# Optimization experiments

Hardware: AMD Instinct MI355X
Metric: run time of the kernel (lower is better)

Reference implementation:

```python
import jax, jax.numpy as jnp
import numpy as np
from jax import lax

B, S, D, H = 8, 1024, 512, 8
K = 25  # moving-average kernel
EPS = 1e-6


def setup_inputs() -> dict:
    key = jax.random.key(0)
    ks = jax.random.split(key, 8)

    def dense_w(k, din, dout):
        return (jax.random.normal(k, (din, dout), jnp.float32) / np.sqrt(din).astype(np.float32))

    return {
        "x": jax.random.normal(ks[0], (B, S, D), jnp.float32),
        "wq": dense_w(ks[1], D, D), "bq": jnp.zeros((D,), jnp.float32),
        "wk": dense_w(ks[2], D, D), "bk": jnp.zeros((D,), jnp.float32),
        "wv": dense_w(ks[3], D, D), "bv": jnp.zeros((D,), jnp.float32),
        "wo": dense_w(ks[4], D, D), "bo": jnp.zeros((D,), jnp.float32),
        "w1": dense_w(ks[5], D, 4 * D), "b1": jnp.zeros((4 * D,), jnp.float32),
        "w2": dense_w(ks[6], 4 * D, D), "b2": jnp.zeros((D,), jnp.float32),
        "g1": jnp.ones((D,), jnp.float32), "be1": jnp.zeros((D,), jnp.float32),
        "g2": jnp.ones((D,), jnp.float32), "be2": jnp.zeros((D,), jnp.float32),
        "g3": jnp.ones((D,), jnp.float32), "be3": jnp.zeros((D,), jnp.float32),
        "num_heads": H,
    }


def _moving_avg(x):
    # TF AveragePooling1D(pool=K, stride=1, padding='same'): divisor excludes padding.
    s = lax.reduce_window(x, 0.0, lax.add, (1, K, 1), (1, 1, 1), 'SAME')
    cnt = lax.reduce_window(jnp.ones((1, x.shape[1], 1), x.dtype), 0.0, lax.add,
                            (1, K, 1), (1, 1, 1), 'SAME')
    return s / cnt


def _layernorm(x, g, b):
    m = jnp.mean(x, -1, keepdims=True)
    v = jnp.var(x, -1, keepdims=True)
    return (x - m) * jax.lax.rsqrt(v + EPS) * g + b


def _auto_correlation(x, wq, bq, wk, bk, wv, bv, wo, bo, num_heads):
    b, s, d = x.shape
    dp = d // num_heads
    def split_heads(t):
        return t.reshape(b, s, num_heads, dp).transpose(0, 2, 1, 3)  # [B,H,S,dp]
    q = split_heads(x @ wq + bq)
    k = split_heads(x @ wk + bk)
    v = split_heads(x @ wv + bv)
    # Faithful to source: rfft over innermost (depth) axis, fft_length = 2*S.
    qf = jnp.fft.rfft(q, n=2 * s, axis=-1)
    kf = jnp.fft.rfft(k, n=2 * s, axis=-1)
    corr = jnp.fft.irfft(qf * jnp.conj(kf), n=2 * s, axis=-1)[..., :s]  # [B,H,S,S]
    scale = 1.0 / np.sqrt(dp).astype(np.float32)
    attn = jax.nn.softmax(scale * corr, axis=-1)
    out = jnp.einsum('bhst,bhtd->bhsd', attn, v)
    out = out.transpose(0, 2, 1, 3).reshape(b, s, d)
    return out @ wo + bo


def reference(x, wq, bq, wk, bk, wv, bv, wo, bo, w1, b1, w2, b2,
              g1, be1, g2, be2, g3, be3, num_heads):
    trend_init = _moving_avg(x)
    seasonal_init = x - trend_init
    attn_out = _auto_correlation(seasonal_init, wq, bq, wk, bk, wv, bv, wo, bo, num_heads)
    out1 = _layernorm(attn_out + seasonal_init, g1, be1)
    ffn = jax.nn.relu(out1 @ w1 + b1) @ w2 + b2
    seasonal_out = _layernorm(out1 + ffn, g2, be2) + seasonal_init
    trend2 = _moving_avg(seasonal_out)
    seasonal_final = seasonal_out - trend2
    x_out = seasonal_final + (trend2 + trend_init)
    return _layernorm(x_out, g3, be3)
```

## Files before the change

### kernel.cpp

```cpp
#include <hip/hip_runtime.h>
#include <cstdint>


typedef float f32x4 __attribute__((ext_vector_type(4)));
typedef __bf16 bf16x8 __attribute__((ext_vector_type(8)));
typedef _Float16 h2t __attribute__((ext_vector_type(2)));
typedef unsigned short u16;
typedef unsigned int u32;
typedef u32 u32x4 __attribute__((ext_vector_type(4)));

__device__ __forceinline__ u16 f2bf(float f) {
  unsigned int u = __float_as_uint(f);
  u = (u + 0x7FFFu + ((u >> 16) & 1u)) >> 16;
  return (u16)u;
}

__device__ __forceinline__ float bf2f(u16 b) { return __uint_as_float((u32)b << 16); }

__device__ __forceinline__ u16 f2h(float f) {
  _Float16 hv = (_Float16)f;
  u16 b;
  __builtin_memcpy(&b, &hv, 2);
  return b;
}

__device__ __forceinline__ float dot2h(u32 qp, u32 kp_, float c) {
#if __has_builtin(__builtin_amdgcn_fdot2)
  return __builtin_amdgcn_fdot2(__builtin_bit_cast(h2t, qp),
                                __builtin_bit_cast(h2t, kp_), c, false);
#else
  h2t q = __builtin_bit_cast(h2t, qp), k = __builtin_bit_cast(h2t, kp_);
  c = fmaf((float)q.x, (float)k.x, c);
  return fmaf((float)q.y, (float)k.y, c);
#endif
}

__device__ __forceinline__ void gload_lds16(const void* g, void* l) {
  __builtin_amdgcn_global_load_lds((__attribute__((address_space(1))) void*)g,
                                   (__attribute__((address_space(3))) void*)l,
                                   16, 0, 0);
}

__global__ __launch_bounds__(256) void movavg_kernel(
    const float* __restrict__ x, u16* __restrict__ seas_bf,
    u16* __restrict__ a64, float* __restrict__ srow) {
  int blk = blockIdx.x;
  int sc = blk & 127, b = blk >> 7;
  int d = threadIdx.x * 2;
  const float* xb = x + (size_t)b * 1024 * 512 + d;
  int s0 = sc * 8;
  int lo = max(s0 - 12, 0), hi = min(s0 + 12, 1023);
  float sx = 0.f, sy = 0.f;
  for (int j = lo; j <= hi; ++j) {
    float2 v = *(const float2*)&xb[(size_t)j * 512];
    sx += v.x;
    sy += v.y;
  }
  float ax = 0.f, ay = 0.f;
#pragma unroll
  for (int s = s0; s < s0 + 8; ++s) {
    int l2 = max(s - 12, 0), h2 = min(s + 12, 1023);
    float invc = 1.f / (float)(h2 - l2 + 1);
    float2 xv = *(const float2*)&xb[(size_t)s * 512];
    float sex = xv.x - sx * invc;
    float sey = xv.y - sy * invc;
    size_t idx = (size_t)(b * 1024 + s) * 512 + d;
    u32 pk = (u32)f2bf(sex) | ((u32)f2bf(sey) << 16);
    *(u32*)&seas_bf[idx] = pk;
    if (s < 64) *(u32*)&a64[(size_t)(b * 64 + s) * 512 + d] = pk;
    ax += sex;
    ay += sey;
    if (s - 12 >= 0) {
      float2 v = *(const float2*)&xb[(size_t)(s - 12) * 512];
      sx -= v.x;
      sy -= v.y;
    }
    if (s + 13 <= 1023) {
      float2 v = *(const float2*)&xb[(size_t)(s + 13) * 512];
      sx += v.x;
      sy += v.y;
    }
  }
  atomicAdd(&srow[b * 512 + d], ax);
  atomicAdd(&srow[b * 512 + d + 1], ay);
}

__global__ __launch_bounds__(256) void weights_prep_kernel(
    const float* __restrict__ wq, const float* __restrict__ wk,
    const float* __restrict__ wv, const float* __restrict__ wo,
    const float* __restrict__ w1, const float* __restrict__ w2,
    const float* __restrict__ bq, const float* __restrict__ bk,
    u16* __restrict__ wqkt, u16* __restrict__ wvt, u16* __restrict__ wot,
    u16* __restrict__ w1t, u16* __restrict__ w2t, float* __restrict__ qkbias) {
  __shared__ float tile[32][33];
  int i = blockIdx.x;
  int tx = threadIdx.x, ty = threadIdx.y;
  if (i >= 3072) {
    int idx = (i - 3072) * 256 + ty * 32 + tx;
    qkbias[idx] = idx < 512 ? bq[idx] : bk[idx - 512];
    return;
  }
  const float* src;
  u16* dst;
  int R, C, bx, by;
  if (i < 1024) {
    int w = i >> 8, l = i & 255;
    src = (w == 0 ? wq : w == 1 ? wk : w == 2 ? wv : wo);
    dst = (w == 0 ? wqkt : w == 1 ? wqkt + 512 * 512 : w == 2 ? wvt : wot);
    R = 512; C = 512; bx = l & 15; by = l >> 4;
  } else if (i < 2048) {
    int l = i - 1024;
    src = w1; dst = w1t; R = 512; C = 2048; bx = l & 15; by = l >> 4;
  } else {
    int l = i - 2048;
    src = w2; dst = w2t; R = 2048; C = 512; bx = l & 63; by = l >> 6;
  }
  int r0 = bx * 32, c0 = by * 32;
#pragma unroll
  for (int k = 0; k < 4; ++k)
    tile[ty + 8 * k][tx] = src[(size_t)(r0 + ty + 8 * k) * C + c0 + tx];
  __syncthreads();
#pragma unroll
  for (int k = 0; k < 4; ++k)
    dst[(size_t)(c0 + ty + 8 * k) * R + r0 + tx] = f2bf(tile[tx][ty + 8 * k]);
}

__global__ __launch_bounds__(256) void vsum_kernel(
    const float* __restrict__ srow, const float* __restrict__ wv,
    const float* __restrict__ bv, float* __restrict__ vsum) {
  int blk = blockIdx.x;
  int b = blk >> 1;
  int n = (blk & 1) * 256 + threadIdx.x;
  float acc = 0.f;
  for (int k = 0; k < 512; ++k) acc += srow[b * 512 + k] * wv[(size_t)k * 512 + n];
  vsum[b * 512 + n] = acc + 1024.f * bv[n];
}

template <int RELU, int OMODE, int KSPLIT>
__global__ __launch_bounds__(256, 6) void gemm_bf16_kernel(
    const u16* __restrict__ A, const u16* __restrict__ Bt,
    const float* __restrict__ bias, void* __restrict__ Cv, void* __restrict__ Cv2,
    int M, int N, int K) {
  constexpr int BK = 32;
  __shared__ u16 As[2][128 * BK];
  __shared__ u16 Bs[2][64 * BK];
  const int tid = threadIdx.x;
  const int wid = tid >> 6, lane = tid & 63;
  const int wm = wid >> 1, wn = wid & 1;
  const int la = lane & 15, lg = lane >> 4;
  int nwg = gridDim.x * gridDim.y;
  int lin = blockIdx.y * gridDim.x + blockIdx.x;
  int swz = (lin & 7) * (nwg >> 3) + (lin >> 3);
  int bx = swz / gridDim.y;
  int by = swz % gridDim.y;
  const int row0 = bx * 128, col0 = by * 64;
  const int z = (KSPLIT > 1) ? (int)blockIdx.z : 0;
  const int kbeg = z * (K / KSPLIT);
  const int ksteps = (K / KSPLIT) / BK;
  f32x4 acc[4][2] = {};

  auto stage = [&](int buf, int k0) {
    {
      int p = tid, r = p >> 2, cg = (p & 3) ^ ((r >> 1) & 3);
      gload_lds16(A + (size_t)(row0 + r) * K + k0 + cg * 8, ((char*)As[buf]) + p * 16);
    }
    {
      int p = tid + 256, r = p >> 2, cg = (p & 3) ^ ((r >> 1) & 3);
      gload_lds16(A + (size_t)(row0 + r) * K + k0 + cg * 8, ((char*)As[buf]) + p * 16);
    }
    {
      int p = tid, r = p >> 2, cg = (p & 3) ^ ((r >> 1) & 3);
      gload_lds16(Bt + (size_t)(col0 + r) * K + k0 + cg * 8, ((char*)Bs[buf]) + p * 16);
    }
  };

  stage(0, kbeg);
  __syncthreads();
  for (int t = 0; t < ksteps; ++t) {
    const int cur = t & 1;
    if (t + 1 < ksteps) stage(cur ^ 1, kbeg + (t + 1) * BK);
    bf16x8 af[4], bfr[2];
#pragma unroll
    for (int m = 0; m < 4; ++m) {
      int r = wm * 64 + m * 16 + la;
      int cp = lg ^ ((r >> 1) & 3);
      af[m] = *(const bf16x8*)(((const char*)As[cur]) + r * 64 + cp * 16);
    }
#pragma unroll
    for (int n = 0; n < 2; ++n) {
      int r = wn * 32 + n * 16 + la;
      int cp = lg ^ ((r >> 1) & 3);
      bfr[n] = *(const bf16x8*)(((const char*)Bs[cur]) + r * 64 + cp * 16);
    }
    __builtin_amdgcn_s_setprio(1);
#pragma unroll
    for (int m = 0; m < 4; ++m)
#pragma unroll
      for (int n = 0; n < 2; ++n)
        acc[m][n] = __builtin_amdgcn_mfma_f32_16x16x32_bf16(af[m], bfr[n], acc[m][n], 0, 0, 0);
    __builtin_amdgcn_s_setprio(0);
    __syncthreads();
  }

  void* Cout = (z == 0) ? Cv : Cv2;
#pragma unroll
  for (int m = 0; m < 4; ++m) {
    int r = row0 + wm * 64 + m * 16 + lg * 4;
#pragma unroll
    for (int n = 0; n < 2; ++n) {
      int cc = col0 + wn * 32 + n * 16 + la;
      float bvv = (z == 0) ? bias[cc] : 0.f;
#pragma unroll
      for (int j = 0; j < 4; ++j) {
        float v = acc[m][n][j] + bvv;
        if (RELU) v = fmaxf(v, 0.f);
        if constexpr (OMODE == 0) {
          ((float*)Cout)[(size_t)(r + j) * N + cc] = v;
        } else if constexpr (OMODE == 1) {
          ((u16*)Cout)[(size_t)(r + j) * N + cc] = f2bf(v);
        } else if constexpr (OMODE == 2) {
          ((u16*)Cout)[(size_t)(r + j) * N + cc] = f2h(v);
        } else {
          int rr = r + j;
          int bb = rr >> 6, tt = rr & 63, hh = cc >> 6, dd = cc & 63;
          ((u16*)Cout)[(((size_t)bb * 8 + hh) * 64 + dd) * 64 + tt] = f2bf(v);
        }
      }
    }
  }
}

__global__ __launch_bounds__(256) void attn_mfma_kernel(
    const u16* __restrict__ qk, const u16* __restrict__ v64t,
    const float* __restrict__ vsum, u16* __restrict__ attn_bf) {
  __shared__ u32 qE[32][64];
  __shared__ u32 qO[32][64];
  __shared__ u32 kp[32][32];
  __shared__ u16 coef[32][64];
  __shared__ u16 vtt[64][64];
  __shared__ float zc[32];
  __shared__ float Vs[64];
  int bid = blockIdx.x;
  int scnk = bid & 31, h = (bid >> 5) & 7, b = bid >> 8;
  int tid = threadIdx.x, wid = tid >> 6, lane = tid & 63;
  int bh = b * 8 + h;

  {
    int p = tid, r = p >> 3, cc = p & 7;
    gload_lds16(v64t + ((size_t)bh * 4096 + r * 64 + ((cc ^ (r & 7)) * 8)),
                ((char*)vtt) + p * 16);
    p = tid + 256; r = p >> 3; cc = p & 7;
    gload_lds16(v64t + ((size_t)bh * 4096 + r * 64 + ((cc ^ (r & 7)) * 8)),
                ((char*)vtt) + p * 16);
  }
  *(f32x4*)&qE[tid >> 3][32 + ((tid & 7) << 2)] = f32x4{};
  {
    int s = tid >> 3, c = tid & 7;
    size_t grow = ((size_t)(b * 1024 + scnk * 32 + s)) * 1024 + h * 64;
    *(f32x4*)&qE[s][c * 4] = *(const f32x4*)&qk[grow + c * 8];
    *(f32x4*)&kp[s][c * 4] = *(const f32x4*)&qk[grow + 512 + c * 8];
  }
  if (tid < 64) Vs[tid] = vsum[b * 512 + h * 64 + tid];
  __syncthreads();
  for (int j2 = tid; j2 < 1024; j2 += 256) {
    int s = j2 >> 5, j = j2 & 31;
    u32 a = qE[s][j], b2 = qE[s][j + 1];
    qO[s][j] = (a >> 16) | (b2 << 16);
    qO[s][j + 32] = 0;
  }
  __syncthreads();
  for (int i = 0; i < 8; ++i) {
    int s = wid * 8 + i;
    u32x4 kk4[8];
#pragma unroll
    for (int u = 0; u < 8; ++u) kk4[u] = *(const u32x4*)&kp[s][u * 4];
    int t = lane, sel = t & 1;
    const u32* qptr = (sel ? qO[s] : qE[s]) + (t >> 1);
    float c = 0.f;
#pragma unroll
    for (int u = 0; u < 8; ++u) {
#pragma unroll
      for (int v = 0; v < 4; ++v) c = dot2h(qptr[u * 4 + v], kk4[u][v], c);
    }
    float sc = c * 0.125f;
    float mx = fmaxf(sc, 0.f);
#pragma unroll
    for (int off = 32; off >= 1; off >>= 1) mx = fmaxf(mx, __shfl_xor(mx, off));
    float w = __expf(sc - mx), wz = __expf(-mx);
    float sw = w;
#pragma unroll
    for (int off = 32; off >= 1; off >>= 1) sw += __shfl_xor(sw, off);
    float inv = 1.f / (sw + 960.f * wz);
    *(u16*)(((char*)&coef[s][0]) + ((2 * t) ^ ((s & 7) << 4))) = f2bf((w - wz) * inv);
    if (lane == 0) zc[s] = wz * inv;
  }
  __syncthreads();
  {
    int sm = wid >> 1, nh = wid & 1;
    int la = lane & 15, lg = lane >> 4;
    int r = sm * 16 + la;
    int n0 = nh * 32 + la, n1 = nh * 32 + 16 + la;
    f32x4 acc0 = {}, acc1 = {};
#pragma unroll
    for (int ks = 0; ks < 2; ++ks) {
      int lr = ks * 4 + lg;
      bf16x8 af = *(const bf16x8*)(((const char*)coef) + r * 128 + ((lr ^ (r & 7)) << 4));
      bf16x8 bf0 = *(const bf16x8*)(((const char*)vtt) + n0 * 128 + ((lr ^ (n0 & 7)) << 4));
      bf16x8 bf1 = *(const bf16x8*)(((const char*)vtt) + n1 * 128 + ((lr ^ (n1 & 7)) << 4));
      acc0 = __builtin_amdgcn_mfma_f32_16x16x32_bf16(af, bf0, acc0, 0, 0, 0);
      acc1 = __builtin_amdgcn_mfma_f32_16x16x32_bf16(af, bf1, acc1, 0, 0, 0);
    }
    int srl0 = sm * 16 + lg * 4;
    int srow0 = b * 1024 + scnk * 32 + srl0;
    float vs0 = Vs[nh * 32 + la], vs1 = Vs[nh * 32 + 16 + la];
#pragma unroll
    for (int j = 0; j < 4; ++j) {
      float zcv = zc[srl0 + j];
      size_t rb = (size_t)(srow0 + j) * 512 + h * 64;
      attn_bf[rb + nh * 32 + la] = f2bf(acc0[j] + zcv * vs0);
      attn_bf[rb + nh * 32 + 16 + la] = f2bf(acc1[j] + zcv * vs1);
    }
  }
}

__device__ __forceinline__ void block_reduce_2(float& a, float& b, float* sbuf) {
  int tid = threadIdx.x, wid = tid >> 6, lane = tid & 63;
#pragma unroll
  for (int off = 32; off >= 1; off >>= 1) {
    a += __shfl_xor(a, off);
    b += __shfl_xor(b, off);
  }
  if (lane == 0) {
    sbuf[wid] = a;
    sbuf[4 + wid] = b;
  }
  __syncthreads();
  a = sbuf[0] + sbuf[1] + sbuf[2] + sbuf[3];
  b = sbuf[4] + sbuf[5] + sbuf[6] + sbuf[7];
  __syncthreads();
}

__global__ __launch_bounds__(256) void ln_res_kernel(
    const u16* __restrict__ xa, const u16* __restrict__ xb,
    u16* __restrict__ res_out,
    const float* __restrict__ g, const float* __restrict__ be) {
  __shared__ float sbuf[8];
  int row = blockIdx.x, tid = threadIdx.x;
  int d = tid * 2;
  size_t base = (size_t)row * 512 + d;
  u32 pa = *(const u32*)&xa[base];
  u32 pb = *(const u32*)&xb[base];
  u32 pr = *(const u32*)&res_out[base];
  float v0 = bf2f((u16)pa) + bf2f((u16)pb) + bf2f((u16)pr);
  float v1 = bf2f((u16)(pa >> 16)) + bf2f((u16)(pb >> 16)) + bf2f((u16)(pr >> 16));
  float s = v0 + v1, q = v0 * v0 + v1 * v1;
  block_reduce_2(s, q, sbuf);
  float mean = s * (1.f / 512.f);
  float var = q * (1.f / 512.f) - mean * mean;
  float rs = rsqrtf(var + 1e-6f);
  float2 gg = *(const float2*)&g[d];
  float2 bb = *(const float2*)&be[d];
  float o0 = (v0 - mean) * rs * gg.x + bb.x;
  float o1 = (v1 - mean) * rs * gg.y + bb.y;
  *(u32*)&res_out[base] = (u32)f2bf(o0) | ((u32)f2bf(o1) << 16);
}

__global__ __launch_bounds__(256) void final_kernel(
    const u16* __restrict__ out1, const u16* __restrict__ fa,
    const u16* __restrict__ fb, const float* __restrict__ x,
    const float* __restrict__ g2, const float* __restrict__ be2,
    const float* __restrict__ g3, const float* __restrict__ be3,
    float* __restrict__ out) {
  __shared__ float sbuf[8];
  int row = blockIdx.x, tid = threadIdx.x;
  int d = tid * 2;
  size_t base = (size_t)row * 512 + d;
  u32 po = *(const u32*)&out1[base];
  u32 pa = *(const u32*)&fa[base];
  u32 pb = *(const u32*)&fb[base];
  float t0 = bf2f((u16)po) + bf2f((u16)pa) + bf2f((u16)pb);
  float t1 = bf2f((u16)(po >> 16)) + bf2f((u16)(pa >> 16)) + bf2f((u16)(pb >> 16));
  float s = t0 + t1, q = t0 * t0 + t1 * t1;
  block_reduce_2(s, q, sbuf);
  float mean = s * (1.f / 512.f);
  float var = q * (1.f / 512.f) - mean * mean;
  float rs = rsqrtf(var + 1e-6f);
  float2 g2v = *(const float2*)&g2[d];
  float2 b2v = *(const float2*)&be2[d];
  float2 xv = *(const float2*)&x[base];
  float y0 = (t0 - mean) * rs * g2v.x + b2v.x + xv.x;
  float y1 = (t1 - mean) * rs * g2v.y + b2v.y + xv.y;
  s = y0 + y1;
  q = y0 * y0 + y1 * y1;
  block_reduce_2(s, q, sbuf);
  mean = s * (1.f / 512.f);
  var = q * (1.f / 512.f) - mean * mean;
  rs = rsqrtf(var + 1e-6f);
  float2 g3v = *(const float2*)&g3[d];
  float2 b3v = *(const float2*)&be3[d];
  float2 o = make_float2((y0 - mean) * rs * g3v.x + b3v.x,
                         (y1 - mean) * rs * g3v.y + b3v.y);
  *(float2*)&out[base] = o;
}

extern "C" void kernel_launch(void* const* d_in, const int* in_sizes, int n_in,
                              void* d_out, int out_size, void* d_ws, size_t ws_size,
                              hipStream_t stream) {
  const float* x = (const float*)d_in[0];
  const float* wq = (const float*)d_in[1];
  const float* bq = (const float*)d_in[2];
  const float* wk = (const float*)d_in[3];
  const float* bk = (const float*)d_in[4];
  const float* wv = (const float*)d_in[5];
  const float* bv = (const float*)d_in[6];
  const float* wo = (const float*)d_in[7];
  const float* bo = (const float*)d_in[8];
  const float* w1 = (const float*)d_in[9];
  const float* b1 = (const float*)d_in[10];
  const float* w2 = (const float*)d_in[11];
  const float* b2 = (const float*)d_in[12];
  const float* g1 = (const float*)d_in[13];
  const float* be1 = (const float*)d_in[14];
  const float* g2 = (const float*)d_in[15];
  const float* be2 = (const float*)d_in[16];
  const float* g3 = (const float*)d_in[17];
  const float* be3 = (const float*)d_in[18];
  float* out = (float*)d_out;

  const size_t MS = 8192ull * 512ull;
  float* srow = (float*)d_ws;
  float* vsumb = srow + 4096;
  float* qkbias = vsumb + 4096;
  u16* qk_f16 = (u16*)(qkbias + 1024);
  u16* hidden = qk_f16 + 8192ull * 1024;
  u16* seas_bf = hidden + 8192ull * 2048;
  u16* attn_bf = seas_bf + MS;
  u16* wo0 = attn_bf + MS;
  u16* wo1 = wo0 + MS;
  u16* v64t = wo1 + MS;
  u16* a64_bf = v64t + 512 * 512;
  u16* wqkt = a64_bf + 512 * 512;
  u16* wvt = wqkt + 1024 * 512;
  u16* wot = wvt + 512 * 512;
  u16* w1t = wot + 512 * 512;
  u16* w2t = w1t + 2048ull * 512;
  u16* ff0 = qk_f16;
  u16* ff1 = ff0 + MS;

  hipMemsetAsync(srow, 0, 4096 * sizeof(float), stream);
  weights_prep_kernel<<<3076, dim3(32, 8), 0, stream>>>(
      wq, wk, wv, wo, w1, w2, bq, bk, wqkt, wvt, wot, w1t, w2t, qkbias);

  movavg_kernel<<<1024, 256, 0, stream>>>(x, seas_bf, a64_bf, srow);
  vsum_kernel<<<16, 256, 0, stream>>>(srow, wv, bv, vsumb);

  gemm_bf16_kernel<0, 2, 1><<<dim3(64, 16), 256, 0, stream>>>(
      seas_bf, wqkt, qkbias, qk_f16, nullptr, 8192, 1024, 512);
  gemm_bf16_kernel<0, 3, 1><<<dim3(4, 8), 256, 0, stream>>>(
      a64_bf, wvt, bv, v64t, nullptr, 512, 512, 512);

  attn_mfma_kernel<<<2048, 256, 0, stream>>>(qk_f16, v64t, vsumb, attn_bf);

  gemm_bf16_kernel<0, 1, 2><<<dim3(64, 8, 2), 256, 0, stream>>>(
      attn_bf, wot, bo, wo0, wo1, 8192, 512, 512);
  ln_res_kernel<<<8192, 256, 0, stream>>>(wo0, wo1, seas_bf, g1, be1);

  gemm_bf16_kernel<1, 1, 1><<<dim3(64, 32), 256, 0, stream>>>(
      seas_bf, w1t, b1, hidden, nullptr, 8192, 2048, 512);
  gemm_bf16_kernel<0, 1, 2><<<dim3(64, 8, 2), 256, 0, stream>>>(
      hidden, w2t, b2, ff0, ff1, 8192, 512, 2048);

  final_kernel<<<8192, 256, 0, stream>>>(seas_bf, ff0, ff1, x, g2, be2, g3, be3, out);
}
```

Before: 214.8 us.

## Replace bf16 GEMMs with 256x128-tile, 8-wave, triple-buffered pipelined kernel

The large GEMMs (QK projection, output projection, FFN up/down) move to a new kernel with 512 threads, 256x128 output tiles, a 64-wide K step split into two 32-wide halves, and a three-stage LDS ring. The ring is managed with explicit vmcnt waits and raw barriers so global-to-LDS loads run two steps ahead of the MFMAs. Larger tiles raise arithmetic intensity and cut redundant operand loads. The cost is fewer workgroups: only 256 blocks for the QK GEMM and 256 for the split-K N=512 GEMMs on a 256-CU part, with one block per CU. The small V GEMM gets its own specialised kernel with the transposed store.

```diff
diff --git a/kernel.cpp b/kernel.cpp
--- a/kernel.cpp
+++ b/kernel.cpp
@@ -137,10 +137,117 @@
 }
 
 template <int RELU, int OMODE, int KSPLIT>
-__global__ __launch_bounds__(256, 6) void gemm_bf16_kernel(
+__global__ __launch_bounds__(512, 1) void gemm8p_kernel(
     const u16* __restrict__ A, const u16* __restrict__ Bt,
     const float* __restrict__ bias, void* __restrict__ Cv, void* __restrict__ Cv2,
     int M, int N, int K) {
+  __shared__ u16 As[3][2][256 * 32];
+  __shared__ u16 Bs[3][2][128 * 32];
+  const int tid = threadIdx.x;
+  const int wid = tid >> 6, lane = tid & 63;
+  const int wm = wid >> 2, wn = wid & 3;
+  const int la = lane & 15, lg = lane >> 4;
+  int nwg = gridDim.x * gridDim.y;
+  int lin = blockIdx.y * gridDim.x + blockIdx.x;
+  int swz = (lin & 7) * (nwg >> 3) + (lin >> 3);
+  int bx = swz / gridDim.y, by = swz % gridDim.y;
+  const int row0 = bx * 256, col0 = by * 128;
+  const int z = (KSPLIT > 1) ? (int)blockIdx.z : 0;
+  const int kbeg = z * (K / KSPLIT);
+  const int nt = (K / KSPLIT) / 64;
+  f32x4 acc[8][2] = {};
+
+  auto stageh = [&](int buf, int h, int k0) {
+    int kh = k0 + h * 32;
+    {
+      int p = tid, r = p >> 2, cg = (p & 3) ^ ((r >> 1) & 3);
+      gload_lds16(A + (size_t)(row0 + r) * K + kh + cg * 8,
+                  ((char*)&As[buf][h][0]) + p * 16);
+    }
+    {
+      int p = tid + 512, r = p >> 2, cg = (p & 3) ^ ((r >> 1) & 3);
+      gload_lds16(A + (size_t)(row0 + r) * K + kh + cg * 8,
+                  ((char*)&As[buf][h][0]) + p * 16);
+    }
+    {
+      int p = tid, r = p >> 2, cg = (p & 3) ^ ((r >> 1) & 3);
+      gload_lds16(Bt + (size_t)(col0 + r) * K + kh + cg * 8,
+                  ((char*)&Bs[buf][h][0]) + p * 16);
+    }
+  };
+
+  stageh(0, 0, kbeg);
+  stageh(0, 1, kbeg);
+  stageh(1, 0, kbeg + 64);
+  stageh(1, 1, kbeg + 64);
+  asm volatile("s_waitcnt vmcnt(6)" ::: "memory");
+  __builtin_amdgcn_s_barrier();
+  __builtin_amdgcn_sched_barrier(0);
+
+  for (int t = 0; t < nt; ++t) {
+    const int buf = t % 3;
+    const int nbuf = (t + 2) % 3;
+    const bool pre = (t + 2 < nt);
+#pragma unroll
+    for (int h = 0; h < 2; ++h) {
+      bf16x8 af[8], bf[2];
+#pragma unroll
+      for (int mf = 0; mf < 8; ++mf) {
+        int r = wm * 128 + mf * 16 + la;
+        int cp = lg ^ ((r >> 1) & 3);
+        af[mf] = *(const bf16x8*)&As[buf][h][r * 32 + cp * 8];
+      }
+#pragma unroll
+      for (int nf = 0; nf < 2; ++nf) {
+        int r = wn * 32 + nf * 16 + la;
+        int cp = lg ^ ((r >> 1) & 3);
+        bf[nf] = *(const bf16x8*)&Bs[buf][h][r * 32 + cp * 8];
+      }
+      if (pre) stageh(nbuf, h, kbeg + (t + 2) * 64);
+      __builtin_amdgcn_sched_barrier(0);
+      __builtin_amdgcn_s_barrier();
+      __builtin_amdgcn_s_setprio(1);
+#pragma unroll
+      for (int mf = 0; mf < 8; ++mf)
+#pragma unroll
+        for (int nf = 0; nf < 2; ++nf)
+          acc[mf][nf] = __builtin_amdgcn_mfma_f32_16x16x32_bf16(af[mf], bf[nf], acc[mf][nf], 0, 0, 0);
+      __builtin_amdgcn_s_setprio(0);
+      __builtin_amdgcn_sched_barrier(0);
+      if (h == 0) __builtin_amdgcn_s_barrier();
+    }
+    if (pre)
+      asm volatile("s_waitcnt vmcnt(6)" ::: "memory");
+    else if (t + 1 < nt)
+      asm volatile("s_waitcnt vmcnt(0)" ::: "memory");
+    __builtin_amdgcn_s_barrier();
+    __builtin_amdgcn_sched_barrier(0);
+  }
+
+  void* Cout = (z == 0) ? Cv : Cv2;
+#pragma unroll
+  for (int mf = 0; mf < 8; ++mf) {
+    int r = row0 + wm * 128 + mf * 16 + lg * 4;
+#pragma unroll
+    for (int nf = 0; nf < 2; ++nf) {
+      int cc = col0 + wn * 32 + nf * 16 + la;
+      float bvv = (z == 0) ? bias[cc] : 0.f;
+#pragma unroll
+      for (int j = 0; j < 4; ++j) {
+        float v = acc[mf][nf][j] + bvv;
+        if (RELU) v = fmaxf(v, 0.f);
+        if constexpr (OMODE == 1)
+          ((u16*)Cout)[(size_t)(r + j) * N + cc] = f2bf(v);
+        else
+          ((u16*)Cout)[(size_t)(r + j) * N + cc] = f2h(v);
+      }
+    }
+  }
+}
+
+__global__ __launch_bounds__(256, 6) void gemm_v_kernel(
+    const u16* __restrict__ A, const u16* __restrict__ Bt,
+    const float* __restrict__ bias, u16* __restrict__ Cv, int M, int N, int K) {
   constexpr int BK = 32;
   __shared__ u16 As[2][128 * BK];
   __shared__ u16 Bs[2][64 * BK];
@@ -148,15 +255,8 @@
   const int wid = tid >> 6, lane = tid & 63;
   const int wm = wid >> 1, wn = wid & 1;
   const int la = lane & 15, lg = lane >> 4;
-  int nwg = gridDim.x * gridDim.y;
-  int lin = blockIdx.y * gridDim.x + blockIdx.x;
-  int swz = (lin & 7) * (nwg >> 3) + (lin >> 3);
-  int bx = swz / gridDim.y;
-  int by = swz % gridDim.y;
-  const int row0 = bx * 128, col0 = by * 64;
-  const int z = (KSPLIT > 1) ? (int)blockIdx.z : 0;
-  const int kbeg = z * (K / KSPLIT);
-  const int ksteps = (K / KSPLIT) / BK;
+  const int row0 = blockIdx.x * 128, col0 = blockIdx.y * 64;
+  const int ksteps = K / BK;
   f32x4 acc[4][2] = {};
 
   auto stage = [&](int buf, int k0) {
@@ -174,11 +274,11 @@
     }
   };
 
-  stage(0, kbeg);
+  stage(0, 0);
   __syncthreads();
   for (int t = 0; t < ksteps; ++t) {
     const int cur = t & 1;
-    if (t + 1 < ksteps) stage(cur ^ 1, kbeg + (t + 1) * BK);
+    if (t + 1 < ksteps) stage(cur ^ 1, (t + 1) * BK);
     bf16x8 af[4], bfr[2];
 #pragma unroll
     for (int m = 0; m < 4; ++m) {
@@ -192,39 +292,27 @@
       int cp = lg ^ ((r >> 1) & 3);
       bfr[n] = *(const bf16x8*)(((const char*)Bs[cur]) + r * 64 + cp * 16);
     }
-    __builtin_amdgcn_s_setprio(1);
 #pragma unroll
     for (int m = 0; m < 4; ++m)
 #pragma unroll
       for (int n = 0; n < 2; ++n)
         acc[m][n] = __builtin_amdgcn_mfma_f32_16x16x32_bf16(af[m], bfr[n], acc[m][n], 0, 0, 0);
-    __builtin_amdgcn_s_setprio(0);
     __syncthreads();
   }
 
-  void* Cout = (z == 0) ? Cv : Cv2;
 #pragma unroll
   for (int m = 0; m < 4; ++m) {
     int r = row0 + wm * 64 + m * 16 + lg * 4;
 #pragma unroll
     for (int n = 0; n < 2; ++n) {
       int cc = col0 + wn * 32 + n * 16 + la;
-      float bvv = (z == 0) ? bias[cc] : 0.f;
+      float bvv = bias[cc];
 #pragma unroll
       for (int j = 0; j < 4; ++j) {
         float v = acc[m][n][j] + bvv;
-        if (RELU) v = fmaxf(v, 0.f);
-        if constexpr (OMODE == 0) {
-          ((float*)Cout)[(size_t)(r + j) * N + cc] = v;
-        } else if constexpr (OMODE == 1) {
-          ((u16*)Cout)[(size_t)(r + j) * N + cc] = f2bf(v);
-        } else if constexpr (OMODE == 2) {
-          ((u16*)Cout)[(size_t)(r + j) * N + cc] = f2h(v);
-        } else {
-          int rr = r + j;
-          int bb = rr >> 6, tt = rr & 63, hh = cc >> 6, dd = cc & 63;
-          ((u16*)Cout)[(((size_t)bb * 8 + hh) * 64 + dd) * 64 + tt] = f2bf(v);
-        }
+        int rr = r + j;
+        int bb = rr >> 6, tt = rr & 63, hh = cc >> 6, dd = cc & 63;
+        Cv[(((size_t)bb * 8 + hh) * 64 + dd) * 64 + tt] = f2bf(v);
       }
     }
   }
@@ -454,20 +542,19 @@
   movavg_kernel<<<1024, 256, 0, stream>>>(x, seas_bf, a64_bf, srow);
   vsum_kernel<<<16, 256, 0, stream>>>(srow, wv, bv, vsumb);
 
-  gemm_bf16_kernel<0, 2, 1><<<dim3(64, 16), 256, 0, stream>>>(
+  gemm8p_kernel<0, 2, 1><<<dim3(32, 8), 512, 0, stream>>>(
       seas_bf, wqkt, qkbias, qk_f16, nullptr, 8192, 1024, 512);
-  gemm_bf16_kernel<0, 3, 1><<<dim3(4, 8), 256, 0, stream>>>(
-      a64_bf, wvt, bv, v64t, nullptr, 512, 512, 512);
+  gemm_v_kernel<<<dim3(4, 8), 256, 0, stream>>>(a64_bf, wvt, bv, v64t, 512, 512, 512);
 
   attn_mfma_kernel<<<2048, 256, 0, stream>>>(qk_f16, v64t, vsumb, attn_bf);
 
-  gemm_bf16_kernel<0, 1, 2><<<dim3(64, 8, 2), 256, 0, stream>>>(
+  gemm8p_kernel<0, 1, 2><<<dim3(32, 4, 2), 512, 0, stream>>>(
       attn_bf, wot, bo, wo0, wo1, 8192, 512, 512);
   ln_res_kernel<<<8192, 256, 0, stream>>>(wo0, wo1, seas_bf, g1, be1);
 
-  gemm_bf16_kernel<1, 1, 1><<<dim3(64, 32), 256, 0, stream>>>(
+  gemm8p_kernel<1, 1, 1><<<dim3(32, 16), 512, 0, stream>>>(
       seas_bf, w1t, b1, hidden, nullptr, 8192, 2048, 512);
-  gemm_bf16_kernel<0, 1, 2><<<dim3(64, 8, 2), 256, 0, stream>>>(
+  gemm8p_kernel<0, 1, 2><<<dim3(32, 4, 2), 512, 0, stream>>>(
       hidden, w2t, b2, ff0, ff1, 8192, 512, 2048);
 
   final_kernel<<<8192, 256, 0, stream>>>(seas_bf, ff0, ff1, x, g2, be2, g3, be3, out);
```

New measurement: 212.3 us. Within noise of the previous version (-1.2%).
